# Performance work log

Hardware: AMD Instinct MI355X
Metric: run time of the kernel (lower is better)

The kernel has to match this reference:

```python
import jax, jax.numpy as jnp
import numpy as np

B, S, F = 8, 2048, 1024
NEG = -1000000000.0

def setup_inputs() -> dict:
    key = jax.random.key(0)
    ks = jax.random.split(key, 8)
    x = jax.random.normal(ks[0], (B, S, F), dtype=jnp.float32)
    # causal attention mask [S, S], 1 = keep, 0 = masked
    attn_mask = jnp.tril(jnp.ones((S, S), dtype=jnp.int32))
    # key padding mask [B, 1, S], random 0/1
    pad_mask = jax.random.randint(ks[1], (B, 1, S), 0, 2, dtype=jnp.int32)
    # ensure at least the first key position is valid per batch to avoid all-masked rows
    pad_mask = pad_mask.at[:, :, 0].set(1)
    sc = 1.0 / np.sqrt(F).astype(np.float32)
    Wq = jax.random.normal(ks[2], (F, F), dtype=jnp.float32) * sc
    bq = jax.random.normal(ks[3], (F,), dtype=jnp.float32) * 0.01
    Wk = jax.random.normal(ks[4], (F, F), dtype=jnp.float32) * sc
    bk = jax.random.normal(ks[5], (F,), dtype=jnp.float32) * 0.01
    Wv = jax.random.normal(ks[6], (F, F), dtype=jnp.float32) * sc
    bv = jax.random.normal(ks[7], (F,), dtype=jnp.float32) * 0.01
    return {"x": x, "attn_mask": attn_mask, "pad_mask": pad_mask,
            "Wq": Wq, "bq": bq, "Wk": Wk, "bk": bk, "Wv": Wv, "bv": bv}

def reference(x, attn_mask, pad_mask, Wq, bq, Wk, bk, Wv, bv):
    # torch Linear: y = x @ W.T + b
    q = jnp.einsum('bsf,of->bso', x, Wq) + bq
    k = jnp.einsum('bsf,of->bso', x, Wk) + bk
    v = jnp.einsum('bsf,of->bso', x, Wv) + bv
    scale = 1.0 / jnp.sqrt(jnp.asarray(q.shape[-1], dtype=x.dtype))
    scores = jnp.einsum('bqf,bkf->bqk', q, k) * scale  # [B, S, S]
    scores = jnp.where(pad_mask == 0, NEG, scores)            # pad_mask [B,1,S] broadcasts
    scores = jnp.where(attn_mask[None, :, :] == 0, NEG, scores)
    prob = jax.nn.softmax(scores, axis=-1)
    # dropout=0.0 (eval / identity)
    return jnp.einsum('bqk,bkf->bqf', prob, v)
```

## Files before the change

kernel.cpp:

```cpp
#include <hip/hip_runtime.h>
#include <hip/hip_bf16.h>
#include <stdint.h>


#define S_LEN 2048
#define F_DIM 1024
#define NBATCH 8
#define BS_TOT (NBATCH * S_LEN)

typedef __attribute__((ext_vector_type(8))) short bf16x8;
typedef __attribute__((ext_vector_type(4))) float f32x4;
typedef unsigned short u16;

__device__ __forceinline__ u16 f32_to_bf16_rne(float f) {
    union { float f; uint32_t u; } v; v.f = f;
    uint32_t u = v.u;
    u += 0x7FFFu + ((u >> 16) & 1u);
    return (u16)(u >> 16);
}
__device__ __forceinline__ float bf16_to_f32(u16 h) {
    union { uint32_t u; float f; } v; v.u = ((uint32_t)h) << 16;
    return v.f;
}

__device__ __forceinline__ void gload_lds16(const u16* g, u16* l) {
    __builtin_amdgcn_global_load_lds(
        (const __attribute__((address_space(1))) void*)g,
        (__attribute__((address_space(3))) void*)l,
        16, 0, 0);
}

__global__ __launch_bounds__(256) void cvt_f32_bf16(const float* __restrict__ in,
                                                    u16* __restrict__ out, int n) {
    int i = (blockIdx.x * 256 + threadIdx.x) * 4;
    if (i + 3 < n) {
        float4 f = *(const float4*)(in + i);
        ushort4 o;
        o.x = f32_to_bf16_rne(f.x); o.y = f32_to_bf16_rne(f.y);
        o.z = f32_to_bf16_rne(f.z); o.w = f32_to_bf16_rne(f.w);
        *(ushort4*)(out + i) = o;
    }
}

__global__ __launch_bounds__(256) void cvt_w3(const float* __restrict__ Wq,
                                              const float* __restrict__ Wk,
                                              const float* __restrict__ Wv,
                                              u16* __restrict__ Wb) {
    const int which = blockIdx.y;
    const float* in = (which == 0) ? Wq : (which == 1) ? Wk : Wv;
    int i = (blockIdx.x * 256 + threadIdx.x) * 4;
    float4 f = *(const float4*)(in + i);
    ushort4 o;
    o.x = f32_to_bf16_rne(f.x); o.y = f32_to_bf16_rne(f.y);
    o.z = f32_to_bf16_rne(f.z); o.w = f32_to_bf16_rne(f.w);
    *(ushort4*)(Wb + (size_t)which * F_DIM * F_DIM + i) = o;
}

template<class Epi>
__device__ __forceinline__ void gemm_tile_128(
    const u16* __restrict__ A, int lda,
    const u16* __restrict__ Bt, int ldb,
    int m0, int n0, int K, float alpha, Epi epi)
{
    __shared__ u16 la[128 * 32];
    __shared__ u16 lb[128 * 32];

    const int tid  = threadIdx.x;
    const int lane = tid & 63;
    const int wave = tid >> 6;
    const int wm = (wave & 1) * 64;
    const int wn = (wave >> 1) * 64;

    f32x4 acc[4][4];
#pragma unroll
    for (int mt = 0; mt < 4; mt++)
#pragma unroll
        for (int nt = 0; nt < 4; nt++)
            acc[mt][nt] = f32x4{0.f, 0.f, 0.f, 0.f};

    const int mrow = wm + (lane & 15);
    const int nrow = wn + (lane & 15);
    const int koff = (lane >> 4) * 8;

    const int cb0 = wave * 64;
    const int cb1 = wave * 64 + 256;
    const int lrow = lane >> 2;
    const int lcol = (lane & 3) * 8;
    const u16* pa0 = A  + (size_t)(m0 + (cb0 >> 2) + lrow) * lda + lcol;
    const u16* pa1 = A  + (size_t)(m0 + (cb1 >> 2) + lrow) * lda + lcol;
    const u16* pb0 = Bt + (size_t)(n0 + (cb0 >> 2) + lrow) * ldb + lcol;
    const u16* pb1 = Bt + (size_t)(n0 + (cb1 >> 2) + lrow) * ldb + lcol;
    u16* qa0 = la + cb0 * 8;
    u16* qa1 = la + cb1 * 8;
    u16* qb0 = lb + cb0 * 8;
    u16* qb1 = lb + cb1 * 8;

    for (int kk = 0; kk < K; kk += 32) {
        __syncthreads();
        gload_lds16(pa0 + kk, qa0);
        gload_lds16(pa1 + kk, qa1);
        gload_lds16(pb0 + kk, qb0);
        gload_lds16(pb1 + kk, qb1);
        __syncthreads();

        bf16x8 fa[4], fb[4];
#pragma unroll
        for (int t = 0; t < 4; t++) {
            fa[t] = *(const bf16x8*)(la + (mrow + t * 16) * 32 + koff);
            fb[t] = *(const bf16x8*)(lb + (nrow + t * 16) * 32 + koff);
        }
#pragma unroll
        for (int mt = 0; mt < 4; mt++)
#pragma unroll
            for (int nt = 0; nt < 4; nt++)
                acc[mt][nt] = __builtin_amdgcn_mfma_f32_16x16x32_bf16(
                    fa[mt], fb[nt], acc[mt][nt], 0, 0, 0);
    }

    const int col   = lane & 15;
    const int rquad = (lane >> 4) * 4;
#pragma unroll
    for (int mt = 0; mt < 4; mt++)
#pragma unroll
        for (int nt = 0; nt < 4; nt++) {
            const int n = n0 + wn + nt * 16 + col;
#pragma unroll
            for (int r = 0; r < 4; r++) {
                const int m = m0 + wm + mt * 16 + rquad + r;
                epi(m, n, acc[mt][nt][r] * alpha);
            }
        }
}

__global__ __launch_bounds__(256) void k_qkv(const u16* __restrict__ xb,
                                             const u16* __restrict__ Wb,
                                             const float* __restrict__ bq,
                                             const float* __restrict__ bk,
                                             const float* __restrict__ bv,
                                             u16* __restrict__ q,
                                             u16* __restrict__ k,
                                             u16* __restrict__ vT) {
    const int which = blockIdx.y;
    const int bx = blockIdx.x;
    const int xcd = bx & 7;
    const int idx = bx >> 3;
    const int m0 = (xcd * 16 + (idx >> 3)) * 128;
    const int n0 = (idx & 7) * 128;
    const float* bias = (which == 0) ? bq : (which == 1) ? bk : bv;
    const u16* W = Wb + (size_t)which * F_DIM * F_DIM;
    if (which < 2) {
        u16* o = (which == 0) ? q : k;
        gemm_tile_128(xb, F_DIM, W, F_DIM, m0, n0, F_DIM, 1.0f,
            [&](int m, int n, float v) {
                o[(size_t)m * F_DIM + n] = f32_to_bf16_rne(v + bias[n]);
            });
    } else {
        gemm_tile_128(xb, F_DIM, W, F_DIM, m0, n0, F_DIM, 1.0f,
            [&](int m, int n, float v) {
                vT[((size_t)(m >> 11) * F_DIM + n) * S_LEN + (m & 2047)] =
                    f32_to_bf16_rne(v + bias[n]);
            });
    }
}

__global__ __launch_bounds__(256) void k_scores(const u16* __restrict__ q,
                                                const u16* __restrict__ k,
                                                const int* __restrict__ pad,
                                                u16* __restrict__ Pp) {
    const int b = blockIdx.x & 7;
    const int t = blockIdx.x >> 3;
    int it = 0, base = 0;
    while (base + it + 1 <= t) { base += it + 1; it++; }
    const int jt = t - base;
    const int* padb = pad + b * S_LEN;
    u16* Pb = Pp + (size_t)b * S_LEN * S_LEN;
    gemm_tile_128(q + (size_t)b * S_LEN * F_DIM, F_DIM,
                  k + (size_t)b * S_LEN * F_DIM, F_DIM,
                  it * 128, jt * 128, F_DIM, 0.03125f,
        [&](int m, int n, float v) {
            u16 o = 0;
            if (n <= m && padb[n] != 0)
                o = f32_to_bf16_rne(__expf(v - 16.0f));
            Pb[(size_t)m * S_LEN + n] = o;
        });
}

__global__ __launch_bounds__(256) void k_rowsum(const u16* __restrict__ Pp,
                                                float* __restrict__ invl) {
    const int wave = threadIdx.x >> 6, lane = threadIdx.x & 63;
    const int r = blockIdx.x * 4 + wave;
    const int b = r >> 11, i = r & 2047;
    const int jlim = ((i >> 7) + 1) << 7;
    const u16* row = Pp + (size_t)b * S_LEN * S_LEN + (size_t)i * S_LEN;
    float s = 0.f;
    for (int j0 = lane * 8; j0 < jlim; j0 += 512) {
        bf16x8 v = *(const bf16x8*)(row + j0);
#pragma unroll
        for (int e = 0; e < 8; e++) s += bf16_to_f32((u16)v[e]);
    }
    for (int off = 32; off > 0; off >>= 1) s += __shfl_xor(s, off);
    if (lane == 0) invl[r] = 1.0f / s;
}

__global__ __launch_bounds__(256) void k_pv(const u16* __restrict__ Pp,
                                            const u16* __restrict__ vT,
                                            const float* __restrict__ invl,
                                            float* __restrict__ out) {
    const int b = blockIdx.x & 7;
    const int rest = blockIdx.x >> 3;
    const int it = rest >> 3;
    const int nt = rest & 7;
    const int Keff = (it + 1) * 128;
    const float* il = invl + b * S_LEN;
    float* ob = out + (size_t)b * S_LEN * F_DIM;
    gemm_tile_128(Pp + (size_t)b * S_LEN * S_LEN, S_LEN,
                  vT + (size_t)b * F_DIM * S_LEN, S_LEN,
                  it * 128, nt * 128, Keff, 1.0f,
        [&](int m, int n, float v) {
            ob[(size_t)m * F_DIM + n] = v * il[m];
        });
}

extern "C" void kernel_launch(void* const* d_in, const int* in_sizes, int n_in,
                              void* d_out, int out_size, void* d_ws, size_t ws_size,
                              hipStream_t stream) {
    const float* x  = (const float*)d_in[0];
    const int* pad  = (const int*)d_in[2];
    const float* Wq = (const float*)d_in[3];
    const float* bq = (const float*)d_in[4];
    const float* Wk = (const float*)d_in[5];
    const float* bk = (const float*)d_in[6];
    const float* Wv = (const float*)d_in[7];
    const float* bv = (const float*)d_in[8];
    float* out = (float*)d_out;

    char* ws = (char*)d_ws;
    u16* q    = (u16*)(ws);
    u16* k    = (u16*)(ws + 32ull * 1024 * 1024);
    u16* vT   = (u16*)(ws + 64ull * 1024 * 1024);
    u16* Pp   = (u16*)(ws + 96ull * 1024 * 1024);
    u16* xb   = (u16*)(ws + 160ull * 1024 * 1024);
    u16* Wb   = (u16*)(ws + 192ull * 1024 * 1024);
    float* il = (float*)(ws + 200ull * 1024 * 1024);

    const int BSF = BS_TOT * F_DIM;
    const int FF = F_DIM * F_DIM;

    cvt_f32_bf16<<<BSF / 1024, 256, 0, stream>>>(x, xb, BSF);
    cvt_w3<<<dim3(FF / 1024, 3), 256, 0, stream>>>(Wq, Wk, Wv, Wb);

    k_qkv<<<dim3(1024, 3), 256, 0, stream>>>(xb, Wb, bq, bk, bv, q, k, vT);

    k_scores<<<1088, 256, 0, stream>>>(q, k, pad, Pp);

    k_rowsum<<<4096, 256, 0, stream>>>(Pp, il);

    k_pv<<<1024, 256, 0, stream>>>(Pp, vT, il, out);
}
```

Before: 408.0 us.

## Fuse softmax row sums into score epilogue and double K-step per barrier

The separate row-sum kernel is removed. Row sums of the exponentiated scores are now accumulated in the score GEMM epilogue through wave shuffles and atomicAdd into a buffer that the weight-convert kernel zeroes. The GEMM core now loads two 32-wide K slabs per barrier pair, halving the number of syncs at the cost of more LDS, and k_pv walks row tiles from longest to shortest to balance its causal load. This saves a full reread of the probability matrix and one launch, but adds atomic traffic and float summation whose order is not deterministic.

```diff
diff --git a/kernel.cpp b/kernel.cpp
--- a/kernel.cpp
+++ b/kernel.cpp
@@ -45,8 +45,13 @@
 __global__ __launch_bounds__(256) void cvt_w3(const float* __restrict__ Wq,
                                               const float* __restrict__ Wk,
                                               const float* __restrict__ Wv,
-                                              u16* __restrict__ Wb) {
+                                              u16* __restrict__ Wb,
+                                              float* __restrict__ lsum) {
     const int which = blockIdx.y;
+    if (which == 0 && blockIdx.x < 16) {
+        const int idx = blockIdx.x * 256 + threadIdx.x;
+        ((float4*)lsum)[idx] = float4{0.f, 0.f, 0.f, 0.f};
+    }
     const float* in = (which == 0) ? Wq : (which == 1) ? Wk : Wv;
     int i = (blockIdx.x * 256 + threadIdx.x) * 4;
     float4 f = *(const float4*)(in + i);
@@ -56,14 +61,15 @@
     *(ushort4*)(Wb + (size_t)which * F_DIM * F_DIM + i) = o;
 }
 
-template<class Epi>
-__device__ __forceinline__ void gemm_tile_128(
+__device__ __forceinline__ void gemm_core_128(
     const u16* __restrict__ A, int lda,
     const u16* __restrict__ Bt, int ldb,
-    int m0, int n0, int K, float alpha, Epi epi)
+    int m0, int n0, int K, f32x4 (&acc)[4][4])
 {
-    __shared__ u16 la[128 * 32];
-    __shared__ u16 lb[128 * 32];
+    __shared__ u16 la0[128 * 32];
+    __shared__ u16 la1[128 * 32];
+    __shared__ u16 lb0[128 * 32];
+    __shared__ u16 lb1[128 * 32];
 
     const int tid  = threadIdx.x;
     const int lane = tid & 63;
@@ -71,7 +77,6 @@
     const int wm = (wave & 1) * 64;
     const int wn = (wave >> 1) * 64;
 
-    f32x4 acc[4][4];
 #pragma unroll
     for (int mt = 0; mt < 4; mt++)
 #pragma unroll
@@ -90,47 +95,39 @@
     const u16* pa1 = A  + (size_t)(m0 + (cb1 >> 2) + lrow) * lda + lcol;
     const u16* pb0 = Bt + (size_t)(n0 + (cb0 >> 2) + lrow) * ldb + lcol;
     const u16* pb1 = Bt + (size_t)(n0 + (cb1 >> 2) + lrow) * ldb + lcol;
-    u16* qa0 = la + cb0 * 8;
-    u16* qa1 = la + cb1 * 8;
-    u16* qb0 = lb + cb0 * 8;
-    u16* qb1 = lb + cb1 * 8;
-
-    for (int kk = 0; kk < K; kk += 32) {
+
+    for (int kk = 0; kk < K; kk += 64) {
         __syncthreads();
-        gload_lds16(pa0 + kk, qa0);
-        gload_lds16(pa1 + kk, qa1);
-        gload_lds16(pb0 + kk, qb0);
-        gload_lds16(pb1 + kk, qb1);
+        gload_lds16(pa0 + kk,      la0 + cb0 * 8);
+        gload_lds16(pa1 + kk,      la0 + cb1 * 8);
+        gload_lds16(pb0 + kk,      lb0 + cb0 * 8);
+        gload_lds16(pb1 + kk,      lb0 + cb1 * 8);
+        gload_lds16(pa0 + kk + 32, la1 + cb0 * 8);
+        gload_lds16(pa1 + kk + 32, la1 + cb1 * 8);
+        gload_lds16(pb0 + kk + 32, lb1 + cb0 * 8);
+        gload_lds16(pb1 + kk + 32, lb1 + cb1 * 8);
         __syncthreads();
 
-        bf16x8 fa[4], fb[4];
-#pragma unroll
-        for (int t = 0; t < 4; t++) {
-            fa[t] = *(const bf16x8*)(la + (mrow + t * 16) * 32 + koff);
-            fb[t] = *(const bf16x8*)(lb + (nrow + t * 16) * 32 + koff);
-        }
-#pragma unroll
-        for (int mt = 0; mt < 4; mt++)
-#pragma unroll
-            for (int nt = 0; nt < 4; nt++)
-                acc[mt][nt] = __builtin_amdgcn_mfma_f32_16x16x32_bf16(
-                    fa[mt], fb[nt], acc[mt][nt], 0, 0, 0);
+#pragma unroll
+        for (int h = 0; h < 2; h++) {
+            const u16* lah = h ? la1 : la0;
+            const u16* lbh = h ? lb1 : lb0;
+            bf16x8 fa[4], fb[4];
+#pragma unroll
+            for (int t = 0; t < 4; t++) {
+                fa[t] = *(const bf16x8*)(lah + (mrow + t * 16) * 32 + koff);
+                fb[t] = *(const bf16x8*)(lbh + (nrow + t * 16) * 32 + koff);
+            }
+#pragma unroll
+            for (int mt = 0; mt < 4; mt++)
+#pragma unroll
+                for (int nt = 0; nt < 4; nt++)
+                    acc[mt][nt] = __builtin_amdgcn_mfma_f32_16x16x32_bf16(
+                        fa[mt], fb[nt], acc[mt][nt], 0, 0, 0);
+        }
     }
-
-    const int col   = lane & 15;
-    const int rquad = (lane >> 4) * 4;
-#pragma unroll
-    for (int mt = 0; mt < 4; mt++)
-#pragma unroll
-        for (int nt = 0; nt < 4; nt++) {
-            const int n = n0 + wn + nt * 16 + col;
-#pragma unroll
-            for (int r = 0; r < 4; r++) {
-                const int m = m0 + wm + mt * 16 + rquad + r;
-                epi(m, n, acc[mt][nt][r] * alpha);
-            }
-        }
-}
+}
+
 
 __global__ __launch_bounds__(256) void k_qkv(const u16* __restrict__ xb,
                                              const u16* __restrict__ Wb,
@@ -148,77 +145,135 @@
     const int n0 = (idx & 7) * 128;
     const float* bias = (which == 0) ? bq : (which == 1) ? bk : bv;
     const u16* W = Wb + (size_t)which * F_DIM * F_DIM;
-    if (which < 2) {
-        u16* o = (which == 0) ? q : k;
-        gemm_tile_128(xb, F_DIM, W, F_DIM, m0, n0, F_DIM, 1.0f,
-            [&](int m, int n, float v) {
-                o[(size_t)m * F_DIM + n] = f32_to_bf16_rne(v + bias[n]);
-            });
-    } else {
-        gemm_tile_128(xb, F_DIM, W, F_DIM, m0, n0, F_DIM, 1.0f,
-            [&](int m, int n, float v) {
-                vT[((size_t)(m >> 11) * F_DIM + n) * S_LEN + (m & 2047)] =
-                    f32_to_bf16_rne(v + bias[n]);
-            });
-    }
+
+    f32x4 acc[4][4];
+    gemm_core_128(xb, F_DIM, W, F_DIM, m0, n0, F_DIM, acc);
+
+    const int lane = threadIdx.x & 63, wave = threadIdx.x >> 6;
+    const int wm = (wave & 1) * 64, wn = (wave >> 1) * 64;
+    const int col = lane & 15, rquad = (lane >> 4) * 4;
+#pragma unroll
+    for (int mt = 0; mt < 4; mt++)
+#pragma unroll
+        for (int nt = 0; nt < 4; nt++) {
+            const int n = n0 + wn + nt * 16 + col;
+            const float badd = bias[n];
+#pragma unroll
+            for (int r = 0; r < 4; r++) {
+                const int m = m0 + wm + mt * 16 + rquad + r;
+                const u16 o = f32_to_bf16_rne(acc[mt][nt][r] + badd);
+                if (which == 0)      q[(size_t)m * F_DIM + n] = o;
+                else if (which == 1) k[(size_t)m * F_DIM + n] = o;
+                else                 vT[((size_t)(m >> 11) * F_DIM + n) * S_LEN + (m & 2047)] = o;
+            }
+        }
 }
 
 __global__ __launch_bounds__(256) void k_scores(const u16* __restrict__ q,
                                                 const u16* __restrict__ k,
                                                 const int* __restrict__ pad,
-                                                u16* __restrict__ Pp) {
+                                                u16* __restrict__ Pp,
+                                                float* __restrict__ lsum) {
     const int b = blockIdx.x & 7;
     const int t = blockIdx.x >> 3;
     int it = 0, base = 0;
     while (base + it + 1 <= t) { base += it + 1; it++; }
     const int jt = t - base;
+    const int m0 = it * 128, n0 = jt * 128;
     const int* padb = pad + b * S_LEN;
     u16* Pb = Pp + (size_t)b * S_LEN * S_LEN;
-    gemm_tile_128(q + (size_t)b * S_LEN * F_DIM, F_DIM,
+    float* lb = lsum + b * S_LEN;
+
+    f32x4 acc[4][4];
+    gemm_core_128(q + (size_t)b * S_LEN * F_DIM, F_DIM,
                   k + (size_t)b * S_LEN * F_DIM, F_DIM,
-                  it * 128, jt * 128, F_DIM, 0.03125f,
-        [&](int m, int n, float v) {
-            u16 o = 0;
-            if (n <= m && padb[n] != 0)
-                o = f32_to_bf16_rne(__expf(v - 16.0f));
-            Pb[(size_t)m * S_LEN + n] = o;
-        });
-}
-
-__global__ __launch_bounds__(256) void k_rowsum(const u16* __restrict__ Pp,
-                                                float* __restrict__ invl) {
-    const int wave = threadIdx.x >> 6, lane = threadIdx.x & 63;
-    const int r = blockIdx.x * 4 + wave;
-    const int b = r >> 11, i = r & 2047;
-    const int jlim = ((i >> 7) + 1) << 7;
-    const u16* row = Pp + (size_t)b * S_LEN * S_LEN + (size_t)i * S_LEN;
-    float s = 0.f;
-    for (int j0 = lane * 8; j0 < jlim; j0 += 512) {
-        bf16x8 v = *(const bf16x8*)(row + j0);
-#pragma unroll
-        for (int e = 0; e < 8; e++) s += bf16_to_f32((u16)v[e]);
-    }
-    for (int off = 32; off > 0; off >>= 1) s += __shfl_xor(s, off);
-    if (lane == 0) invl[r] = 1.0f / s;
+                  m0, n0, F_DIM, acc);
+
+    const int lane = threadIdx.x & 63, wave = threadIdx.x >> 6;
+    const int wm = (wave & 1) * 64, wn = (wave >> 1) * 64;
+    const int col = lane & 15, rquad = (lane >> 4) * 4;
+
+    int pv[4];
+#pragma unroll
+    for (int nt = 0; nt < 4; nt++) pv[nt] = padb[n0 + wn + nt * 16 + col];
+
+    float rs[4][4];
+#pragma unroll
+    for (int mt = 0; mt < 4; mt++)
+#pragma unroll
+        for (int r = 0; r < 4; r++) rs[mt][r] = 0.f;
+
+#pragma unroll
+    for (int mt = 0; mt < 4; mt++)
+#pragma unroll
+        for (int nt = 0; nt < 4; nt++) {
+            const int n = n0 + wn + nt * 16 + col;
+#pragma unroll
+            for (int r = 0; r < 4; r++) {
+                const int m = m0 + wm + mt * 16 + rquad + r;
+                u16 o = 0;
+                if (n <= m && pv[nt] != 0) {
+                    o = f32_to_bf16_rne(__expf(acc[mt][nt][r] * 0.03125f - 16.0f));
+                    rs[mt][r] += bf16_to_f32(o);
+                }
+                Pb[(size_t)m * S_LEN + n] = o;
+            }
+        }
+
+#pragma unroll
+    for (int mt = 0; mt < 4; mt++)
+#pragma unroll
+        for (int r = 0; r < 4; r++) {
+            float s = rs[mt][r];
+            s += __shfl_xor(s, 1);
+            s += __shfl_xor(s, 2);
+            s += __shfl_xor(s, 4);
+            s += __shfl_xor(s, 8);
+            if (col == 0)
+                atomicAdd(&lb[wm + mt * 16 + rquad + r + m0], s);
+        }
 }
 
 __global__ __launch_bounds__(256) void k_pv(const u16* __restrict__ Pp,
                                             const u16* __restrict__ vT,
-                                            const float* __restrict__ invl,
+                                            const float* __restrict__ lsum,
                                             float* __restrict__ out) {
     const int b = blockIdx.x & 7;
     const int rest = blockIdx.x >> 3;
-    const int it = rest >> 3;
-    const int nt = rest & 7;
+    const int it = 15 - (rest >> 3);
+    const int nt4 = rest & 7;
     const int Keff = (it + 1) * 128;
-    const float* il = invl + b * S_LEN;
+    const int m0 = it * 128, n0 = nt4 * 128;
+    const float* lb = lsum + b * S_LEN;
     float* ob = out + (size_t)b * S_LEN * F_DIM;
-    gemm_tile_128(Pp + (size_t)b * S_LEN * S_LEN, S_LEN,
+
+    f32x4 acc[4][4];
+    gemm_core_128(Pp + (size_t)b * S_LEN * S_LEN, S_LEN,
                   vT + (size_t)b * F_DIM * S_LEN, S_LEN,
-                  it * 128, nt * 128, Keff, 1.0f,
-        [&](int m, int n, float v) {
-            ob[(size_t)m * F_DIM + n] = v * il[m];
-        });
+                  m0, n0, Keff, acc);
+
+    const int lane = threadIdx.x & 63, wave = threadIdx.x >> 6;
+    const int wm = (wave & 1) * 64, wn = (wave >> 1) * 64;
+    const int col = lane & 15, rquad = (lane >> 4) * 4;
+
+    float inv[4][4];
+#pragma unroll
+    for (int mt = 0; mt < 4; mt++)
+#pragma unroll
+        for (int r = 0; r < 4; r++)
+            inv[mt][r] = 1.0f / lb[m0 + wm + mt * 16 + rquad + r];
+
+#pragma unroll
+    for (int mt = 0; mt < 4; mt++)
+#pragma unroll
+        for (int nt = 0; nt < 4; nt++) {
+            const int n = n0 + wn + nt * 16 + col;
+#pragma unroll
+            for (int r = 0; r < 4; r++) {
+                const int m = m0 + wm + mt * 16 + rquad + r;
+                ob[(size_t)m * F_DIM + n] = acc[mt][nt][r] * inv[mt][r];
+            }
+        }
 }
 
 extern "C" void kernel_launch(void* const* d_in, const int* in_sizes, int n_in,
@@ -247,13 +302,11 @@
     const int FF = F_DIM * F_DIM;
 
     cvt_f32_bf16<<<BSF / 1024, 256, 0, stream>>>(x, xb, BSF);
-    cvt_w3<<<dim3(FF / 1024, 3), 256, 0, stream>>>(Wq, Wk, Wv, Wb);
+    cvt_w3<<<dim3(FF / 1024, 3), 256, 0, stream>>>(Wq, Wk, Wv, Wb, il);
 
     k_qkv<<<dim3(1024, 3), 256, 0, stream>>>(xb, Wb, bq, bk, bv, q, k, vT);
 
-    k_scores<<<1088, 256, 0, stream>>>(q, k, pad, Pp);
-
-    k_rowsum<<<4096, 256, 0, stream>>>(Pp, il);
+    k_scores<<<1088, 256, 0, stream>>>(q, k, pad, Pp, il);
 
     k_pv<<<1024, 256, 0, stream>>>(Pp, vT, il, out);
 }
```

Measured after the change: 437.2 us. 7.1% more time.
